# Performance work log

Hardware: AMD Instinct MI355X
Metric: run time of the kernel (lower is better)

The kernel has to match this reference:

```python
import jax, jax.numpy as jnp
import numpy as np

B, Hs, Ws, ENC = 128, 14, 14, 2048
ATT, EMB, DEC, V, L = 512, 512, 512, 30000, 22


def setup_inputs() -> dict:
    key = jax.random.key(0)
    ks = jax.random.split(key, 16)
    u = lambda k, shape, a: jax.random.uniform(k, shape, jnp.float32, -a, a)
    cap_len_rest = jax.random.randint(ks[2], (B - 1, 1), 2, L + 1)
    caption_lengths = jnp.concatenate([jnp.array([[L]], dtype=cap_len_rest.dtype), cap_len_rest], axis=0)
    return {
        "encoder_out": jax.random.normal(ks[0], (B, Hs, Ws, ENC), jnp.float32),
        "encoded_captions": jax.random.randint(ks[1], (B, L), 0, V),
        "caption_lengths": caption_lengths,
        # learned parameters
        "emb_table": u(ks[3], (V, EMB), 0.1),
        "We": u(ks[4], (ENC, ATT), 0.02), "be": jnp.zeros((ATT,), jnp.float32),
        "Wd": u(ks[5], (DEC, ATT), 0.02), "bd": jnp.zeros((ATT,), jnp.float32),
        "wf": u(ks[6], (ATT,), 0.02), "bf": jnp.zeros((), jnp.float32),
        "W_ih": u(ks[7], (4 * DEC, EMB + ENC), 0.02), "b_ih": jnp.zeros((4 * DEC,), jnp.float32),
        "W_hh": u(ks[8], (4 * DEC, DEC), 0.02), "b_hh": jnp.zeros((4 * DEC,), jnp.float32),
        "W_fc": u(ks[9], (DEC, V), 0.1), "b_fc": jnp.zeros((V,), jnp.float32),
    }


def reference(encoder_out, encoded_captions, caption_lengths,
              emb_table, We, be, Wd, bd, wf, bf,
              W_ih, b_ih, W_hh, b_hh, W_fc, b_fc):
    Bsz = encoder_out.shape[0]
    enc = encoder_out.reshape(Bsz, -1, encoder_out.shape[-1])  # [B, P, ENC]
    lens = caption_lengths[:, 0]
    sort_ind = jnp.argsort(-lens)  # descending, stable
    lens = lens[sort_ind]
    enc = enc[sort_ind]
    caps = encoded_captions[sort_ind]
    emb = emb_table[caps]  # [B, L, EMB]
    dec_lens = lens - 1
    T = caps.shape[1] - 1  # static max(decode_lengths) (max length present in batch)
    D = W_hh.shape[1]

    attn1 = enc @ We + be  # [B, P, ATT], loop-invariant
    h0 = jnp.zeros((Bsz, D), enc.dtype)
    c0 = jnp.zeros((Bsz, D), enc.dtype)

    def step(carry, xs):
        h, c = carry
        emb_t, active = xs  # [B, EMB], [B] bool
        attn2 = h @ Wd + bd  # [B, ATT]
        e = jnp.einsum('bpa,a->bp', jax.nn.relu(attn1 + attn2[:, None, :]), wf) + bf
        alpha = jax.nn.softmax(e, axis=1)  # [B, P]
        ctx = jnp.einsum('bp,bpe->be', alpha, enc)  # [B, ENC]
        x = jnp.concatenate([emb_t, ctx], axis=1)
        gates = x @ W_ih.T + b_ih + h @ W_hh.T + b_hh
        i, f, g, o = jnp.split(gates, 4, axis=1)  # PyTorch LSTM gate order
        c_new = jax.nn.sigmoid(f) * c + jax.nn.sigmoid(i) * jnp.tanh(g)
        h_new = jax.nn.sigmoid(o) * jnp.tanh(c_new)
        m = active[:, None]
        h = jnp.where(m, h_new, h)
        c = jnp.where(m, c_new, c)
        out_t = jnp.where(m, h_new @ W_fc + b_fc, 0.0)  # [B, V]
        alpha_t = jnp.where(m, alpha, 0.0)
        return (h, c), (out_t, alpha_t)

    ts = jnp.arange(T)
    active = ts[:, None] < dec_lens[None, :]  # [T, B]
    emb_steps = jnp.transpose(emb[:, :T], (1, 0, 2))  # [T, B, EMB]
    (_, _), (outs, alphas) = jax.lax.scan(step, (h0, c0), (emb_steps, active))
    outputs = jnp.transpose(outs, (1, 0, 2))  # [B, T, V]
    alphas = jnp.transpose(alphas, (1, 0, 2))  # [B, T, P]
    return outputs, caps, dec_lens, alphas, sort_ind
```

## Files before the change

### kernel.cpp

```cpp
#include <hip/hip_runtime.h>
#include <cstdint>
#include <cstddef>

#define B_    128
#define P_    196
#define ENC_  2048
#define ATT_  512
#define DEC_  512
#define EMB_  512
#define V_    30000
#define VPAD_ 30080
#define L_    22
#define T_    21
#define KGATE (EMB_ + ENC_ + DEC_)
#define NGATE (4*DEC_)
#define KS    8
#define LDSK  40

typedef unsigned short u16;
typedef unsigned int   u32;
typedef float f32x4 __attribute__((ext_vector_type(4)));
typedef short s16x8 __attribute__((ext_vector_type(8)));

__device__ __forceinline__ u16 f2bf(float f){
  u32 u = __float_as_uint(f);
  u = (u + 0x7fffu + ((u >> 16) & 1u)) >> 16;
  return (u16)u;
}
__device__ __forceinline__ float bf2f(u16 h){
  return __uint_as_float(((u32)h) << 16);
}

__device__ __forceinline__ void gload_lds16(const u16* g, u16* l){
  __builtin_amdgcn_global_load_lds(
      (const __attribute__((address_space(1))) void*)g,
      (__attribute__((address_space(3))) void*)l, 16, 0, 0);
}

template<int MODE>
__global__ __launch_bounds__(256)
void gemm_bt(const u16* __restrict__ A,
             const u16* __restrict__ Bt,
             int N, int K,
             const float* __restrict__ bias,
             u16* __restrict__ outb,
             float* __restrict__ outp,
             const int* __restrict__ declens)
{
  __shared__ __align__(16) u16 As[128*32];
  __shared__ __align__(16) u16 Bs[128*32];
  __shared__ __align__(16) float Cs[32*132];

  const int tid = threadIdx.x;
  const int bxn = (MODE == 2) ? blockIdx.y : blockIdx.x;
  const int bym = (MODE == 2) ? blockIdx.x : blockIdx.y;
  const int nt = bxn * 128;
  const size_t mt = (size_t)bym * 128;

  const int wv = tid >> 6;
  const int ln = tid & 63;
  const int lm = ln & 15;
  const int qd = ln >> 4;
  const int wr = wv >> 1;
  const int wc = wv & 1;

  f32x4 acc[4][4];
  #pragma unroll
  for (int i=0;i<4;i++)
    #pragma unroll
    for (int j=0;j<4;j++) acc[i][j] = f32x4{0.f,0.f,0.f,0.f};

  const int c0 = tid, c1 = 256 + tid;
  const int ar0 = c0 >> 2, ac0 = (((c0 & 3) ^ ((ar0 >> 1) & 3)) * 8);
  const int ar1 = c1 >> 2, ac1 = (((c1 & 3) ^ ((ar1 >> 1) & 3)) * 8);
  const u16* Ab0 = A  + (mt + ar0) * (size_t)K + ac0;
  const u16* Ab1 = A  + (mt + ar1) * (size_t)K + ac1;
  const u16* Bb0 = Bt + ((size_t)nt + ar0) * (size_t)K + ac0;
  const u16* Bb1 = Bt + ((size_t)nt + ar1) * (size_t)K + ac1;
  u16* lA0 = As + (size_t)c0 * 8;
  u16* lA1 = As + (size_t)c1 * 8;
  u16* lB0 = Bs + (size_t)c0 * 8;
  u16* lB1 = Bs + (size_t)c1 * 8;

  int aoff[4], boff[4];
  #pragma unroll
  for (int i=0;i<4;i++){
    int ra = wr*64 + i*16 + lm;
    aoff[i] = ra*32 + ((qd ^ ((ra >> 1) & 3)) * 8);
    int rb = wc*64 + i*16 + lm;
    boff[i] = rb*32 + ((qd ^ ((rb >> 1) & 3)) * 8);
  }

  for (int kc = 0; kc < K; kc += 32){
    gload_lds16(Ab0 + kc, lA0);
    gload_lds16(Ab1 + kc, lA1);
    gload_lds16(Bb0 + kc, lB0);
    gload_lds16(Bb1 + kc, lB1);
    __syncthreads();
    s16x8 af[4], bfr[4];
    #pragma unroll
    for (int i=0;i<4;i++) af[i]  = *reinterpret_cast<const s16x8*>(As + aoff[i]);
    #pragma unroll
    for (int i=0;i<4;i++) bfr[i] = *reinterpret_cast<const s16x8*>(Bs + boff[i]);
    #pragma unroll
    for (int i=0;i<4;i++)
      #pragma unroll
      for (int j=0;j<4;j++)
        acc[i][j] = __builtin_amdgcn_mfma_f32_16x16x32_bf16(af[i], bfr[j], acc[i][j], 0, 0, 0);
    __syncthreads();
  }

  #pragma unroll
  for (int mi=0; mi<4; mi++){
    const int lrb = wr*16 + qd*4;
    #pragma unroll
    for (int ni=0; ni<4; ni++)
      #pragma unroll
      for (int rr=0; rr<4; rr++)
        Cs[(lrb+rr)*132 + wc*64 + ni*16 + lm] = acc[mi][ni][rr];
    __syncthreads();
    const int er = tid >> 3;
    const int ec = (tid & 7) * 16;
    const size_t grow = mt + (size_t)(er >> 4)*64 + mi*16 + (er & 15);
    const float* cr = Cs + er*132 + ec;
    if (MODE == 0){
      __align__(16) u16 pk[16];
      #pragma unroll
      for (int j=0;j<16;j++) pk[j] = f2bf(cr[j] + bias[nt + ec + j]);
      uint4* dst = reinterpret_cast<uint4*>(outb + grow*(size_t)N + nt + ec);
      dst[0] = *reinterpret_cast<uint4*>(pk);
      dst[1] = *reinterpret_cast<uint4*>(pk + 8);
    } else {
      const int ti = (int)(grow >> 7);
      const int bb = (int)(grow & 127);
      const bool act = ti < declens[bb];
      float* dst = outp + ((size_t)bb*T_ + ti)*(size_t)V_ + nt + ec;
      if (nt + 128 <= N){
        #pragma unroll
        for (int j=0;j<4;j++){
          float4 v;
          v.x = act ? cr[4*j+0] + bias[nt+ec+4*j+0] : 0.f;
          v.y = act ? cr[4*j+1] + bias[nt+ec+4*j+1] : 0.f;
          v.z = act ? cr[4*j+2] + bias[nt+ec+4*j+2] : 0.f;
          v.w = act ? cr[4*j+3] + bias[nt+ec+4*j+3] : 0.f;
          reinterpret_cast<float4*>(dst)[j] = v;
        }
      } else {
        #pragma unroll
        for (int j=0;j<16;j++){
          int col = nt + ec + j;
          if (col < N) dst[j] = act ? cr[j] + bias[col] : 0.f;
        }
      }
    }
    __syncthreads();
  }
}

template<int MODE>
__global__ __launch_bounds__(256)
void gemm_bf16(const u16* __restrict__ A, int lda,
               const u16* __restrict__ Bm, int N, int K, int M,
               const float* __restrict__ bias,
               u16* __restrict__ outb,
               float* __restrict__ outp,
               const int* __restrict__ declens)
{
  __shared__ __align__(16) u16 As[64*LDSK];
  __shared__ __align__(16) u16 Bs[64*LDSK];
  __shared__ __align__(16) float Cs[64*68];

  const int tid = threadIdx.x;
  const int nt = blockIdx.x * 64;
  const int mt = blockIdx.y * 64;
  int k0 = 0, k1 = K;
  if (MODE == 1){ int kl = K / KS; k0 = blockIdx.z * kl; k1 = k0 + kl; }

  f32x4 acc[4];
  #pragma unroll
  for (int s = 0; s < 4; s++) acc[s] = f32x4{0.f,0.f,0.f,0.f};

  const int am = tid >> 2;
  const int ak = (tid & 3) * 8;
  const int bk = tid >> 3;
  const int bn = (tid & 7) * 8;
  const int wv = tid >> 6;
  const int ln = tid & 63;
  const int qd = ln >> 4;
  const int lm = ln & 15;

  for (int kc = k0; kc < k1; kc += 32){
    uint4 av = *reinterpret_cast<const uint4*>(A + (size_t)(mt + am) * lda + kc + ak);
    *reinterpret_cast<uint4*>(&As[am * LDSK + ak]) = av;
    u16 bv[8];
    uint4 bq = *reinterpret_cast<const uint4*>(Bm + (size_t)(kc + bk) * N + nt + bn);
    bv[0]=(u16)(bq.x&0xffff); bv[1]=(u16)(bq.x>>16);
    bv[2]=(u16)(bq.y&0xffff); bv[3]=(u16)(bq.y>>16);
    bv[4]=(u16)(bq.z&0xffff); bv[5]=(u16)(bq.z>>16);
    bv[6]=(u16)(bq.w&0xffff); bv[7]=(u16)(bq.w>>16);
    #pragma unroll
    for (int j=0;j<8;j++) Bs[(bn + j) * LDSK + bk] = bv[j];
    __syncthreads();

    s16x8 af = *reinterpret_cast<const s16x8*>(&As[(wv*16 + lm) * LDSK + qd*8]);
    #pragma unroll
    for (int s=0;s<4;s++){
      s16x8 bfr = *reinterpret_cast<const s16x8*>(&Bs[(s*16 + lm) * LDSK + qd*8]);
      acc[s] = __builtin_amdgcn_mfma_f32_16x16x32_bf16(af, bfr, acc[s], 0, 0, 0);
    }
    __syncthreads();
  }

  #pragma unroll
  for (int s=0;s<4;s++)
    #pragma unroll
    for (int r=0;r<4;r++)
      Cs[(wv*16 + qd*4 + r)*68 + s*16 + lm] = acc[s][r];
  __syncthreads();

  const int row = tid >> 2;
  const int cs0 = (tid & 3) * 16;
  if (MODE == 1){
    float* dst = outp + (size_t)blockIdx.z * M * N + (size_t)(mt+row)*N + nt + cs0;
    #pragma unroll
    for (int j=0;j<4;j++){
      float4 v = { Cs[row*68+cs0+4*j], Cs[row*68+cs0+4*j+1],
                   Cs[row*68+cs0+4*j+2], Cs[row*68+cs0+4*j+3] };
      reinterpret_cast<float4*>(dst)[j] = v;
    }
  }
}

__global__ void cvt_bf16(const float* __restrict__ in, u16* __restrict__ out, int n4){
  int i = blockIdx.x * blockDim.x + threadIdx.x;
  int stride = gridDim.x * blockDim.x;
  for (; i < n4; i += stride){
    float4 v = reinterpret_cast<const float4*>(in)[i];
    __align__(8) u16 p[4] = {f2bf(v.x), f2bf(v.y), f2bf(v.z), f2bf(v.w)};
    reinterpret_cast<uint2*>(out)[i] = *reinterpret_cast<uint2*>(p);
  }
}

__global__ void transpose_cvt(const float* __restrict__ in, u16* __restrict__ out,
                              int K, int N)
{
  __shared__ float tile[32][33];
  int n0 = blockIdx.x * 32, k0 = blockIdx.y * 32;
  int tx = threadIdx.x, ty = threadIdx.y;
  #pragma unroll
  for (int j=0;j<4;j++){
    int k = k0 + ty + j*8, n = n0 + tx;
    tile[ty + j*8][tx] = (n < N) ? in[(size_t)k*N + n] : 0.f;
  }
  __syncthreads();
  #pragma unroll
  for (int j=0;j<4;j++){
    int nl = ty + j*8;
    out[(size_t)(n0 + nl)*K + k0 + tx] = f2bf(tile[tx][nl]);
  }
}

__global__ void build_bigb(const float* __restrict__ Wih, const float* __restrict__ Whh,
                           u16* __restrict__ out)
{
  __shared__ float tile[32][33];
  int k0 = blockIdx.x * 32, n0 = blockIdx.y * 32;
  int tx = threadIdx.x, ty = threadIdx.y;
  #pragma unroll
  for (int j=0;j<4;j++){
    int nl = ty + j*8;
    int n = n0 + nl, k = k0 + tx;
    float v = (k0 < 2560) ? Wih[(size_t)n*2560 + k] : Whh[(size_t)n*512 + (k - 2560)];
    tile[nl][tx] = v;
  }
  __syncthreads();
  #pragma unroll
  for (int j=0;j<4;j++){
    int kl = ty + j*8;
    out[(size_t)(k0 + kl)*NGATE + n0 + tx] = f2bf(tile[tx][kl]);
  }
}

__global__ void sort_kernel(const int* __restrict__ cap_len, const int* __restrict__ caps,
                            int* __restrict__ sortind, int* __restrict__ declens,
                            int* __restrict__ caps_s,
                            float* __restrict__ out_caps, float* __restrict__ out_declens,
                            float* __restrict__ out_sortind)
{
  __shared__ int si[B_];
  if (threadIdx.x == 0){
    int cnt = 0;
    for (int v = L_; v >= 0 && cnt < B_; v--)
      for (int b = 0; b < B_; b++)
        if (cap_len[b] == v) si[cnt++] = b;
  }
  __syncthreads();
  for (int i = threadIdx.x; i < B_; i += 256){
    int sb = si[i];
    sortind[i] = sb; out_sortind[i] = (float)sb;
    int dl = cap_len[sb] - 1;
    declens[i] = dl; out_declens[i] = (float)dl;
  }
  for (int i = threadIdx.x; i < B_*L_; i += 256){
    int bb = i / L_;
    int c = caps[si[bb]*L_ + (i % L_)];
    caps_s[i] = c; out_caps[i] = (float)c;
  }
}

__global__ void emb_fill(const float* __restrict__ emb_table, const int* __restrict__ caps_i,
                         u16* __restrict__ xa, int t)
{
  int b = blockIdx.x;
  int cap = caps_i[b*L_ + t];
  for (int k = threadIdx.x; k < EMB_; k += 256)
    xa[(size_t)b*KGATE + k] = f2bf(emb_table[(size_t)cap*EMB_ + k]);
}

__global__ __launch_bounds__(256)
void attn_esm(const u16* __restrict__ attn1, const float* __restrict__ a2part,
              const float* __restrict__ bd, const float* __restrict__ wf,
              const float* __restrict__ bfp,
              const int* __restrict__ sortind, const int* __restrict__ declens,
              float* __restrict__ alpha_buf, float* __restrict__ out_alphas, int t)
{
  __shared__ float a2[ATT_];
  __shared__ float wfs[ATT_];
  __shared__ float es[P_];
  __shared__ float red[8];
  int b = blockIdx.x, tid = threadIdx.x;
  for (int i = tid; i < ATT_; i += 256){
    float v = bd[i];
    #pragma unroll
    for (int s=0;s<KS;s++) v += a2part[((size_t)s*B_ + b)*ATT_ + i];
    a2[i] = v;
    wfs[i] = wf[i];
  }
  __syncthreads();
  int sb = sortind[b];
  const u16* arow = attn1 + (size_t)sb * P_ * ATT_;
  int wv = tid >> 6, ln = tid & 63;
  float bfv = bfp[0];
  for (int i = 0; i < P_/4; i++){
    int p = i*4 + wv;
    uint4 q = *reinterpret_cast<const uint4*>(arow + (size_t)p*ATT_ + ln*8);
    u32 wd_[4] = {q.x, q.y, q.z, q.w};
    float sum = 0.f;
    #pragma unroll
    for (int j=0;j<4;j++){
      int a0 = ln*8 + 2*j;
      float v0 = bf2f((u16)(wd_[j] & 0xffff)) + a2[a0];
      float v1 = bf2f((u16)(wd_[j] >> 16))    + a2[a0+1];
      sum += fmaxf(v0, 0.f) * wfs[a0];
      sum += fmaxf(v1, 0.f) * wfs[a0+1];
    }
    #pragma unroll
    for (int off=32; off; off>>=1) sum += __shfl_xor(sum, off);
    if (ln == 0) es[p] = sum + bfv;
  }
  __syncthreads();
  float m = (tid < P_) ? es[tid] : -1e30f;
  #pragma unroll
  for (int off=32; off; off>>=1) m = fmaxf(m, __shfl_xor(m, off));
  if (ln == 0) red[wv] = m;
  __syncthreads();
  m = fmaxf(fmaxf(red[0],red[1]), fmaxf(red[2],red[3]));
  float ev = (tid < P_) ? expf(es[tid] - m) : 0.f;
  float sm = ev;
  #pragma unroll
  for (int off=32; off; off>>=1) sm += __shfl_xor(sm, off);
  if (ln == 0) red[4+wv] = sm;
  __syncthreads();
  float tot = red[4]+red[5]+red[6]+red[7];
  if (tid < P_){
    float al = ev / tot;
    alpha_buf[b*P_ + tid] = al;
    out_alphas[((size_t)b*T_ + t)*P_ + tid] = (t < declens[b]) ? al : 0.f;
  }
}

__global__ __launch_bounds__(256)
void ctx_kernel(const u16* __restrict__ enc_bf, const float* __restrict__ alpha_buf,
                const int* __restrict__ sortind, u16* __restrict__ xa)
{
  __shared__ float al[P_];
  int b = blockIdx.x, ch = blockIdx.y, tid = threadIdx.x;
  for (int i = tid; i < P_; i += 256) al[i] = alpha_buf[b*P_ + i];
  __syncthreads();
  int sb = sortind[b];
  const u16* eb = enc_bf + (size_t)sb * P_ * ENC_ + ch * 1024 + tid * 4;
  float a0=0.f, a1=0.f, a2v=0.f, a3=0.f;
  #pragma unroll 4
  for (int p=0;p<P_;p++){
    uint2 q = *reinterpret_cast<const uint2*>(eb + (size_t)p * ENC_);
    float w = al[p];
    a0  += w * bf2f((u16)(q.x & 0xffff));
    a1  += w * bf2f((u16)(q.x >> 16));
    a2v += w * bf2f((u16)(q.y & 0xffff));
    a3  += w * bf2f((u16)(q.y >> 16));
  }
  __align__(8) u16 pk[4] = {f2bf(a0), f2bf(a1), f2bf(a2v), f2bf(a3)};
  *reinterpret_cast<uint2*>(xa + (size_t)b*KGATE + EMB_ + ch*1024 + tid*4) =
      *reinterpret_cast<uint2*>(pk);
}

__global__ __launch_bounds__(256)
void lstm_kernel(const float* __restrict__ gpart, const float* __restrict__ bih,
                 const float* __restrict__ bhh,
                 float* __restrict__ hf, float* __restrict__ cfb,
                 u16* __restrict__ xa, u16* __restrict__ Hh,
                 const int* __restrict__ declens, const int* __restrict__ caps_i,
                 const float* __restrict__ emb_table, int t)
{
  int b = blockIdx.x, tid = threadIdx.x;
  bool act = t < declens[b];
  #pragma unroll
  for (int j=0;j<2;j++){
    int n = j*256 + tid;
    float gi = bih[n]      + bhh[n];
    float gf = bih[n+512]  + bhh[n+512];
    float gg = bih[n+1024] + bhh[n+1024];
    float go = bih[n+1536] + bhh[n+1536];
    #pragma unroll
    for (int s=0;s<KS;s++){
      const float* gp = gpart + ((size_t)s*B_ + b)*NGATE;
      gi += gp[n]; gf += gp[n+512]; gg += gp[n+1024]; go += gp[n+1536];
    }
    float co = cfb[b*DEC_ + n];
    float iv = 1.f/(1.f + expf(-gi));
    float fv = 1.f/(1.f + expf(-gf));
    float gv = tanhf(gg);
    float ov = 1.f/(1.f + expf(-go));
    float cn = fv*co + iv*gv;
    float hn = ov * tanhf(cn);
    float ho = act ? hn : hf[b*DEC_ + n];
    float c2 = act ? cn : co;
    hf[b*DEC_ + n] = ho;
    cfb[b*DEC_ + n] = c2;
    u16 hb = f2bf(ho);
    xa[(size_t)b*KGATE + EMB_ + ENC_ + n] = hb;
    Hh[((size_t)t*B_ + b)*DEC_ + n] = hb;
  }
  if (t + 1 < T_){
    int cap = caps_i[b*L_ + t + 1];
    for (int k = tid; k < EMB_; k += 256)
      xa[(size_t)b*KGATE + k] = f2bf(emb_table[(size_t)cap*EMB_ + k]);
  }
}

extern "C" void kernel_launch(void* const* d_in, const int* in_sizes, int n_in,
                              void* d_out, int out_size, void* d_ws, size_t ws_size,
                              hipStream_t stream)
{
  (void)in_sizes; (void)n_in; (void)out_size; (void)ws_size;
  const float* enc  = (const float*)d_in[0];
  const int*   caps = (const int*)d_in[1];
  const int*   clen = (const int*)d_in[2];
  const float* embt = (const float*)d_in[3];
  const float* We   = (const float*)d_in[4];
  const float* be   = (const float*)d_in[5];
  const float* Wd   = (const float*)d_in[6];
  const float* bd   = (const float*)d_in[7];
  const float* wf   = (const float*)d_in[8];
  const float* bfp  = (const float*)d_in[9];
  const float* Wih  = (const float*)d_in[10];
  const float* bih  = (const float*)d_in[11];
  const float* Whh  = (const float*)d_in[12];
  const float* bhh  = (const float*)d_in[13];
  const float* Wfc  = (const float*)d_in[14];
  const float* bfc  = (const float*)d_in[15];

  float* out = (float*)d_out;
  float* out_outputs = out;
  float* out_caps    = out + (size_t)80640000;
  float* out_declens = out + (size_t)80640000 + 2816;
  float* out_alphas  = out + (size_t)80640000 + 2816 + 128;
  float* out_sortind = out + (size_t)80640000 + 2816 + 128 + 526848;

  char* w = (char*)d_ws;
  size_t off = 0;
  auto alloc = [&](size_t bytes)->char*{
    char* p = w + off; off += (bytes + 255) & ~(size_t)255; return p;
  };
  u16*  enc_bf = (u16*)alloc((size_t)B_*P_*ENC_*2);
  u16*  attn1  = (u16*)alloc((size_t)B_*P_*ATT_*2);
  u16*  WeT    = (u16*)alloc((size_t)ATT_*ENC_*2);
  u16*  Wd_bf  = (u16*)alloc((size_t)DEC_*ATT_*2);
  u16*  BigB   = (u16*)alloc((size_t)KGATE*NGATE*2);
  u16*  WfcT   = (u16*)alloc((size_t)VPAD_*DEC_*2);
  u16*  Hh     = (u16*)alloc((size_t)T_*B_*DEC_*2);
  float* hf    = (float*)alloc((size_t)B_*DEC_*4);
  float* cf    = (float*)alloc((size_t)B_*DEC_*4);
  u16*  xa     = (u16*)alloc((size_t)B_*KGATE*2);
  float* a2p   = (float*)alloc((size_t)KS*B_*ATT_*4);
  float* gp    = (float*)alloc((size_t)KS*B_*NGATE*4);
  float* albuf = (float*)alloc((size_t)B_*P_*4);
  int*  caps_i = (int*)alloc((size_t)B_*L_*4);
  int*  decl_i = (int*)alloc(512);
  int*  sort_i = (int*)alloc(512);

  hipMemsetAsync(hf, 0, (size_t)B_*DEC_*4*2 + (size_t)B_*KGATE*2, stream);

  sort_kernel<<<1, 256, 0, stream>>>(clen, caps, sort_i, decl_i, caps_i,
                                     out_caps, out_declens, out_sortind);
  emb_fill<<<B_, 256, 0, stream>>>(embt, caps_i, xa, 0);

  cvt_bf16<<<4096, 256, 0, stream>>>(enc, enc_bf, (int)((size_t)B_*P_*ENC_/4));
  cvt_bf16<<<128, 256, 0, stream>>>(Wd, Wd_bf, DEC_*ATT_/4);
  transpose_cvt<<<dim3(ATT_/32, ENC_/32), dim3(32, 8), 0, stream>>>(We, WeT, ENC_, ATT_);
  transpose_cvt<<<dim3(VPAD_/32, DEC_/32), dim3(32, 8), 0, stream>>>(Wfc, WfcT, DEC_, V_);
  build_bigb<<<dim3(KGATE/32, NGATE/32), dim3(32, 8), 0, stream>>>(Wih, Whh, BigB);

  gemm_bt<0><<<dim3(ATT_/128, (B_*P_)/128), 256, 0, stream>>>(
      enc_bf, WeT, ATT_, ENC_, be, attn1, nullptr, nullptr);

  for (int t = 0; t < T_; t++){
    gemm_bf16<1><<<dim3(ATT_/64, B_/64, KS), 256, 0, stream>>>(
        xa + EMB_ + ENC_, KGATE, Wd_bf, ATT_, DEC_, B_, nullptr, nullptr, a2p, nullptr);
    attn_esm<<<B_, 256, 0, stream>>>(attn1, a2p, bd, wf, bfp, sort_i, decl_i,
                                     albuf, out_alphas, t);
    ctx_kernel<<<dim3(B_, 2), 256, 0, stream>>>(enc_bf, albuf, sort_i, xa);
    gemm_bf16<1><<<dim3(NGATE/64, B_/64, KS), 256, 0, stream>>>(
        xa, KGATE, BigB, NGATE, KGATE, B_, nullptr, nullptr, gp, nullptr);
    lstm_kernel<<<B_, 256, 0, stream>>>(gp, bih, bhh, hf, cf, xa, Hh,
                                        decl_i, caps_i, embt, t);
  }

  gemm_bt<2><<<dim3((T_*B_)/128, VPAD_/128), 256, 0, stream>>>(
      Hh, WfcT, V_, DEC_, bfc, nullptr, out_outputs, decl_i);
}
```

Measured before the change: 2.643 ms.

## Fuse attention decoder projection into LSTM kernel, double-buffer GEMM, remap tiles for XCDs

The per-step h@Wd split-K GEMM launch is removed and computed inside lstm_kernel from the new hidden state in shared memory, writing a dense a2 buffer that attn_esm reads directly. The generic gemm_bt gains double-buffered LDS staging so the next K tile loads while MFMAs run, and its block index is remapped so neighbouring tiles land on the same XCD. ctx_kernel is split into four column chunks per batch row instead of two, raising parallelism. The fused matvec has each of 128 blocks read the full Wd matrix, and the larger LDS footprint in gemm_bt may reduce occupancy.

```diff
diff --git a/kernel.cpp b/kernel.cpp
--- a/kernel.cpp
+++ b/kernel.cpp
@@ -47,13 +47,23 @@
              float* __restrict__ outp,
              const int* __restrict__ declens)
 {
-  __shared__ __align__(16) u16 As[128*32];
-  __shared__ __align__(16) u16 Bs[128*32];
-  __shared__ __align__(16) float Cs[32*132];
+  __shared__ __align__(16) char smem[32768];
+  u16 (*As)[128*32] = reinterpret_cast<u16(*)[128*32]>(smem);
+  u16 (*Bs)[128*32] = reinterpret_cast<u16(*)[128*32]>(smem + 16384);
+  float* Cs = reinterpret_cast<float*>(smem);
 
   const int tid = threadIdx.x;
-  const int bxn = (MODE == 2) ? blockIdx.y : blockIdx.x;
-  const int bym = (MODE == 2) ? blockIdx.x : blockIdx.y;
+
+  const int nwg = gridDim.x * gridDim.y;
+  int lin = blockIdx.y * gridDim.x + blockIdx.x;
+  {
+    int q = nwg >> 3, r = nwg & 7;
+    int xcd = lin & 7, idx = lin >> 3;
+    lin = (xcd < r ? xcd * (q + 1) : r * (q + 1) + (xcd - r) * q) + idx;
+  }
+  int bxn, bym;
+  if (MODE == 2){ bym = lin % gridDim.x; bxn = lin / gridDim.x; }
+  else          { bxn = lin % gridDim.x; bym = lin / gridDim.x; }
   const int nt = bxn * 128;
   const size_t mt = (size_t)bym * 128;
 
@@ -77,10 +87,7 @@
   const u16* Ab1 = A  + (mt + ar1) * (size_t)K + ac1;
   const u16* Bb0 = Bt + ((size_t)nt + ar0) * (size_t)K + ac0;
   const u16* Bb1 = Bt + ((size_t)nt + ar1) * (size_t)K + ac1;
-  u16* lA0 = As + (size_t)c0 * 8;
-  u16* lA1 = As + (size_t)c1 * 8;
-  u16* lB0 = Bs + (size_t)c0 * 8;
-  u16* lB1 = Bs + (size_t)c1 * 8;
+  const int lo0 = c0 * 8, lo1 = c1 * 8;
 
   int aoff[4], boff[4];
   #pragma unroll
@@ -91,24 +98,32 @@
     boff[i] = rb*32 + ((qd ^ ((rb >> 1) & 3)) * 8);
   }
 
+#define STAGE_(buf, kc) do {                       \
+    gload_lds16(Ab0 + (kc), &As[buf][lo0]);        \
+    gload_lds16(Ab1 + (kc), &As[buf][lo1]);        \
+    gload_lds16(Bb0 + (kc), &Bs[buf][lo0]);        \
+    gload_lds16(Bb1 + (kc), &Bs[buf][lo1]);        \
+  } while(0)
+
+  STAGE_(0, 0);
+  __syncthreads();
+  int cur = 0;
   for (int kc = 0; kc < K; kc += 32){
-    gload_lds16(Ab0 + kc, lA0);
-    gload_lds16(Ab1 + kc, lA1);
-    gload_lds16(Bb0 + kc, lB0);
-    gload_lds16(Bb1 + kc, lB1);
-    __syncthreads();
+    if (kc + 32 < K) STAGE_(cur ^ 1, kc + 32);
     s16x8 af[4], bfr[4];
     #pragma unroll
-    for (int i=0;i<4;i++) af[i]  = *reinterpret_cast<const s16x8*>(As + aoff[i]);
-    #pragma unroll
-    for (int i=0;i<4;i++) bfr[i] = *reinterpret_cast<const s16x8*>(Bs + boff[i]);
+    for (int i=0;i<4;i++) af[i]  = *reinterpret_cast<const s16x8*>(&As[cur][aoff[i]]);
+    #pragma unroll
+    for (int i=0;i<4;i++) bfr[i] = *reinterpret_cast<const s16x8*>(&Bs[cur][boff[i]]);
     #pragma unroll
     for (int i=0;i<4;i++)
       #pragma unroll
       for (int j=0;j<4;j++)
         acc[i][j] = __builtin_amdgcn_mfma_f32_16x16x32_bf16(af[i], bfr[j], acc[i][j], 0, 0, 0);
     __syncthreads();
-  }
+    cur ^= 1;
+  }
+#undef STAGE_
 
   #pragma unroll
   for (int mi=0; mi<4; mi++){
@@ -318,7 +333,7 @@
 }
 
 __global__ __launch_bounds__(256)
-void attn_esm(const u16* __restrict__ attn1, const float* __restrict__ a2part,
+void attn_esm(const u16* __restrict__ attn1, const float* __restrict__ a2dense,
               const float* __restrict__ bd, const float* __restrict__ wf,
               const float* __restrict__ bfp,
               const int* __restrict__ sortind, const int* __restrict__ declens,
@@ -330,10 +345,7 @@
   __shared__ float red[8];
   int b = blockIdx.x, tid = threadIdx.x;
   for (int i = tid; i < ATT_; i += 256){
-    float v = bd[i];
-    #pragma unroll
-    for (int s=0;s<KS;s++) v += a2part[((size_t)s*B_ + b)*ATT_ + i];
-    a2[i] = v;
+    a2[i] = bd[i] + a2dense[(size_t)b*ATT_ + i];
     wfs[i] = wf[i];
   }
   __syncthreads();
@@ -388,20 +400,18 @@
   for (int i = tid; i < P_; i += 256) al[i] = alpha_buf[b*P_ + i];
   __syncthreads();
   int sb = sortind[b];
-  const u16* eb = enc_bf + (size_t)sb * P_ * ENC_ + ch * 1024 + tid * 4;
-  float a0=0.f, a1=0.f, a2v=0.f, a3=0.f;
-  #pragma unroll 4
+  const u16* eb = enc_bf + (size_t)sb * P_ * ENC_ + ch * 512 + tid * 2;
+  float a0=0.f, a1=0.f;
+  #pragma unroll 8
   for (int p=0;p<P_;p++){
-    uint2 q = *reinterpret_cast<const uint2*>(eb + (size_t)p * ENC_);
+    u32 q = *reinterpret_cast<const u32*>(eb + (size_t)p * ENC_);
     float w = al[p];
-    a0  += w * bf2f((u16)(q.x & 0xffff));
-    a1  += w * bf2f((u16)(q.x >> 16));
-    a2v += w * bf2f((u16)(q.y & 0xffff));
-    a3  += w * bf2f((u16)(q.y >> 16));
-  }
-  __align__(8) u16 pk[4] = {f2bf(a0), f2bf(a1), f2bf(a2v), f2bf(a3)};
-  *reinterpret_cast<uint2*>(xa + (size_t)b*KGATE + EMB_ + ch*1024 + tid*4) =
-      *reinterpret_cast<uint2*>(pk);
+    a0 += w * bf2f((u16)(q & 0xffff));
+    a1 += w * bf2f((u16)(q >> 16));
+  }
+  __align__(4) u16 pk[2] = {f2bf(a0), f2bf(a1)};
+  *reinterpret_cast<u32*>(xa + (size_t)b*KGATE + EMB_ + ch*512 + tid*2) =
+      *reinterpret_cast<u32*>(pk);
 }
 
 __global__ __launch_bounds__(256)
@@ -410,8 +420,10 @@
                  float* __restrict__ hf, float* __restrict__ cfb,
                  u16* __restrict__ xa, u16* __restrict__ Hh,
                  const int* __restrict__ declens, const int* __restrict__ caps_i,
-                 const float* __restrict__ emb_table, int t)
-{
+                 const float* __restrict__ emb_table,
+                 const u16* __restrict__ WdT, float* __restrict__ a2buf, int t)
+{
+  __shared__ float hs[DEC_];
   int b = blockIdx.x, tid = threadIdx.x;
   bool act = t < declens[b];
   #pragma unroll
@@ -440,11 +452,29 @@
     u16 hb = f2bf(ho);
     xa[(size_t)b*KGATE + EMB_ + ENC_ + n] = hb;
     Hh[((size_t)t*B_ + b)*DEC_ + n] = hb;
+    hs[n] = bf2f(hb);
   }
   if (t + 1 < T_){
     int cap = caps_i[b*L_ + t + 1];
     for (int k = tid; k < EMB_; k += 256)
       xa[(size_t)b*KGATE + k] = f2bf(emb_table[(size_t)cap*EMB_ + k]);
+    __syncthreads();
+    #pragma unroll
+    for (int j=0;j<2;j++){
+      int a = j*256 + tid;
+      const u16* wr = WdT + (size_t)a * DEC_;
+      float s = 0.f;
+      for (int k=0;k<DEC_;k+=8){
+        uint4 q = *reinterpret_cast<const uint4*>(wr + k);
+        u32 ww[4] = {q.x, q.y, q.z, q.w};
+        #pragma unroll
+        for (int u2=0;u2<4;u2++){
+          s += bf2f((u16)(ww[u2] & 0xffff)) * hs[k + 2*u2];
+          s += bf2f((u16)(ww[u2] >> 16))    * hs[k + 2*u2 + 1];
+        }
+      }
+      a2buf[(size_t)b*ATT_ + a] = s;
+    }
   }
 }
 
@@ -485,29 +515,30 @@
   u16*  enc_bf = (u16*)alloc((size_t)B_*P_*ENC_*2);
   u16*  attn1  = (u16*)alloc((size_t)B_*P_*ATT_*2);
   u16*  WeT    = (u16*)alloc((size_t)ATT_*ENC_*2);
-  u16*  Wd_bf  = (u16*)alloc((size_t)DEC_*ATT_*2);
+  u16*  WdT    = (u16*)alloc((size_t)ATT_*DEC_*2);
   u16*  BigB   = (u16*)alloc((size_t)KGATE*NGATE*2);
   u16*  WfcT   = (u16*)alloc((size_t)VPAD_*DEC_*2);
   u16*  Hh     = (u16*)alloc((size_t)T_*B_*DEC_*2);
   float* hf    = (float*)alloc((size_t)B_*DEC_*4);
   float* cf    = (float*)alloc((size_t)B_*DEC_*4);
   u16*  xa     = (u16*)alloc((size_t)B_*KGATE*2);
-  float* a2p   = (float*)alloc((size_t)KS*B_*ATT_*4);
+  float* a2buf = (float*)alloc((size_t)B_*ATT_*4);
   float* gp    = (float*)alloc((size_t)KS*B_*NGATE*4);
   float* albuf = (float*)alloc((size_t)B_*P_*4);
   int*  caps_i = (int*)alloc((size_t)B_*L_*4);
   int*  decl_i = (int*)alloc(512);
   int*  sort_i = (int*)alloc(512);
 
-  hipMemsetAsync(hf, 0, (size_t)B_*DEC_*4*2 + (size_t)B_*KGATE*2, stream);
+  hipMemsetAsync(hf, 0,
+      (size_t)B_*DEC_*4*2 + (size_t)B_*KGATE*2 + (size_t)B_*ATT_*4, stream);
 
   sort_kernel<<<1, 256, 0, stream>>>(clen, caps, sort_i, decl_i, caps_i,
                                      out_caps, out_declens, out_sortind);
   emb_fill<<<B_, 256, 0, stream>>>(embt, caps_i, xa, 0);
 
   cvt_bf16<<<4096, 256, 0, stream>>>(enc, enc_bf, (int)((size_t)B_*P_*ENC_/4));
-  cvt_bf16<<<128, 256, 0, stream>>>(Wd, Wd_bf, DEC_*ATT_/4);
   transpose_cvt<<<dim3(ATT_/32, ENC_/32), dim3(32, 8), 0, stream>>>(We, WeT, ENC_, ATT_);
+  transpose_cvt<<<dim3(ATT_/32, DEC_/32), dim3(32, 8), 0, stream>>>(Wd, WdT, DEC_, ATT_);
   transpose_cvt<<<dim3(VPAD_/32, DEC_/32), dim3(32, 8), 0, stream>>>(Wfc, WfcT, DEC_, V_);
   build_bigb<<<dim3(KGATE/32, NGATE/32), dim3(32, 8), 0, stream>>>(Wih, Whh, BigB);
 
@@ -515,15 +546,13 @@
       enc_bf, WeT, ATT_, ENC_, be, attn1, nullptr, nullptr);
 
   for (int t = 0; t < T_; t++){
-    gemm_bf16<1><<<dim3(ATT_/64, B_/64, KS), 256, 0, stream>>>(
-        xa + EMB_ + ENC_, KGATE, Wd_bf, ATT_, DEC_, B_, nullptr, nullptr, a2p, nullptr);
-    attn_esm<<<B_, 256, 0, stream>>>(attn1, a2p, bd, wf, bfp, sort_i, decl_i,
+    attn_esm<<<B_, 256, 0, stream>>>(attn1, a2buf, bd, wf, bfp, sort_i, decl_i,
                                      albuf, out_alphas, t);
-    ctx_kernel<<<dim3(B_, 2), 256, 0, stream>>>(enc_bf, albuf, sort_i, xa);
+    ctx_kernel<<<dim3(B_, 4), 256, 0, stream>>>(enc_bf, albuf, sort_i, xa);
     gemm_bf16<1><<<dim3(NGATE/64, B_/64, KS), 256, 0, stream>>>(
         xa, KGATE, BigB, NGATE, KGATE, B_, nullptr, nullptr, gp, nullptr);
     lstm_kernel<<<B_, 256, 0, stream>>>(gp, bih, bhh, hf, cf, xa, Hh,
-                                        decl_i, caps_i, embt, t);
+                                        decl_i, caps_i, embt, WdT, a2buf, t);
   }
 
   gemm_bt<2><<<dim3((T_*B_)/128, VPAD_/128), 256, 0, stream>>>(
```

Result: slower. 2.930 ms (+10.9%).
